# Kernel tuning notes

Hardware: AMD Instinct MI355X
Metric: run time of the kernel (lower is better)

The kernel has to match this reference:

```python
import jax, jax.numpy as jnp
import numpy as np
import math

EMBED_DIM = 1024
NUM_HEADS = 16
HEAD_DIM = EMBED_DIM // NUM_HEADS


def setup_inputs() -> dict:
    key = jax.random.key(0)
    ks = jax.random.split(key, 9)
    B, S, D = 4, 2048, EMBED_DIM
    s = 1.0 / math.sqrt(D)
    x = jax.random.normal(ks[0], (B, S, D), dtype=jnp.float32)
    Wq = jax.random.normal(ks[1], (D, D), dtype=jnp.float32) * s
    bq = jnp.zeros((D,), dtype=jnp.float32)
    Wk = jax.random.normal(ks[2], (D, D), dtype=jnp.float32) * s
    bk = jnp.zeros((D,), dtype=jnp.float32)
    Wv = jax.random.normal(ks[3], (D, D), dtype=jnp.float32) * s
    bv = jnp.zeros((D,), dtype=jnp.float32)
    Wo = jax.random.normal(ks[4], (D, D), dtype=jnp.float32) * s
    bo = jnp.zeros((D,), dtype=jnp.float32)
    return {"x": x, "Wq": Wq, "bq": bq, "Wk": Wk, "bk": bk,
            "Wv": Wv, "bv": bv, "Wo": Wo, "bo": bo}


def reference(x, Wq, bq, Wk, bk, Wv, bv, Wo, bo):
    B, S, D = x.shape
    H, hd = NUM_HEADS, HEAD_DIM
    # projections: [B,S,D] -> [B,H,S,hd]
    def split_heads(t):
        return t.reshape(B, S, H, hd).transpose(0, 2, 1, 3)
    Q = split_heads(x @ Wq + bq)
    K = split_heads(x @ Wk + bk)
    V = split_heads(x @ Wv + bv)
    scale = 1.0 / math.sqrt(hd)
    scores = jnp.einsum('bhqd,bhkd->bhqk', Q, K) * scale  # [B,H,S,S]
    causal = jnp.tril(jnp.ones((S, S), dtype=bool))
    scores = jnp.where(causal, scores, -jnp.inf)
    attn = jax.nn.softmax(scores, axis=-1)
    out = jnp.einsum('bhqk,bhkd->bhqd', attn, V)  # [B,H,S,hd]
    out = out.transpose(0, 2, 1, 3).reshape(B, S, D)
    return out @ Wo + bo
```

## Files before the change

kernel.cpp:

```cpp
#include <hip/hip_runtime.h>
#include <hip/hip_bf16.h>
#include <cstdint>
#include <cstddef>

typedef __bf16 bf16_t;
typedef __bf16 bf16x4 __attribute__((ext_vector_type(4)));
typedef __bf16 bf16x8 __attribute__((ext_vector_type(8)));
typedef float f32x4 __attribute__((ext_vector_type(4)));
typedef float f32x16 __attribute__((ext_vector_type(16)));
typedef unsigned u32x2 __attribute__((ext_vector_type(2)));

typedef __attribute__((address_space(1))) void as1_void_t;
typedef __attribute__((address_space(3))) void as3_void_t;

__device__ __forceinline__ void gload_lds16(const bf16_t* g, bf16_t* l) {
  __builtin_amdgcn_global_load_lds((as1_void_t*)g, (as3_void_t*)l, 16, 0, 0);
}

__global__ __launch_bounds__(256) void prep_x_k(
    const float* __restrict__ x, bf16_t* __restrict__ xb)
{
  const int stride = gridDim.x * blockDim.x;
  const int tid = blockIdx.x * blockDim.x + threadIdx.x;
  const int NX4 = (8192 * 1024) / 4;
  for (int i = tid; i < NX4; i += stride) {
    float4 v = ((const float4*)x)[i];
    bf16x4 o;
    o[0] = (bf16_t)v.x; o[1] = (bf16_t)v.y; o[2] = (bf16_t)v.z; o[3] = (bf16_t)v.w;
    ((bf16x4*)xb)[i] = o;
  }
}

__global__ __launch_bounds__(256) void prep_w_k(
    const float* __restrict__ wq, const float* __restrict__ wk,
    const float* __restrict__ wv, const float* __restrict__ wo,
    bf16_t* __restrict__ wqt, bf16_t* __restrict__ wkt,
    bf16_t* __restrict__ wvt, bf16_t* __restrict__ wot)
{
  __shared__ float t[64][65];
  const int zz = blockIdx.y;
  const float* w = (zz == 0) ? wq : (zz == 1) ? wk : (zz == 2) ? wv : wo;
  bf16_t* wt = (zz == 0) ? wqt : (zz == 1) ? wkt : (zz == 2) ? wvt : wot;
  const int tile = blockIdx.x;
  const int tr = tile >> 4, tc = tile & 15;
  const int c = threadIdx.x & 63, r4 = threadIdx.x >> 6;
#pragma unroll
  for (int rr = 0; rr < 16; ++rr) {
    int row = rr * 4 + r4;
    t[row][c] = w[(size_t)(tr * 64 + row) * 1024 + tc * 64 + c];
  }
  __syncthreads();
#pragma unroll
  for (int rr = 0; rr < 16; ++rr) {
    int row = rr * 4 + r4;
    wt[(size_t)(tc * 64 + row) * 1024 + tr * 64 + c] = (bf16_t)t[c][row];
  }
}

constexpr int BM = 128, BN = 128, BK = 64;

__global__ __launch_bounds__(256) void gemm_qkv_k(
    const bf16_t* __restrict__ A,
    const bf16_t* __restrict__ WqT, const bf16_t* __restrict__ WkT,
    const bf16_t* __restrict__ WvT,
    const float* __restrict__ bq, const float* __restrict__ bk,
    const float* __restrict__ bv,
    bf16_t* __restrict__ qo, bf16_t* __restrict__ ko, bf16_t* __restrict__ vo)
{
  constexpr int K = 1024;
  __shared__ bf16_t a_lds[BM * BK];
  __shared__ bf16_t b_lds[BN * BK];
  const int z = blockIdx.z;
  const bf16_t* Bt = (z == 0) ? WqT : (z == 1) ? WkT : WvT;
  const float* bias = (z == 0) ? bq : (z == 1) ? bk : bv;
  bf16_t* outp = (z == 0) ? qo : (z == 1) ? ko : vo;
  const float oscale = (z == 0) ? 0.18033688011112042f : 1.0f;

  const int tid = threadIdx.x;
  const int l = tid & 63;
  const int wv = tid >> 6;
  const int wr = wv >> 1, wc = wv & 1;
  const int lr = l & 15, lg = l >> 4;
  const int bm = blockIdx.x * BM;
  const int bn = blockIdx.y * BN;

  f32x4 acc[4][4] = {};

  const int srow = tid >> 3;
  const int scc = tid & 7;

  for (int k0 = 0; k0 < K; k0 += BK) {
    __syncthreads();
#pragma unroll
    for (int it = 0; it < 4; ++it) {
      int row = srow + it * 32;
      int gk = (scc ^ (row & 7)) * 8;
      gload_lds16(A + (size_t)(bm + row) * K + k0 + gk, a_lds + row * BK + scc * 8);
      gload_lds16(Bt + (size_t)(bn + row) * K + k0 + gk, b_lds + row * BK + scc * 8);
    }
    __syncthreads();
#pragma unroll
    for (int kk = 0; kk < 2; ++kk) {
      bf16x8 af[4], bfr[4];
#pragma unroll
      for (int m = 0; m < 4; ++m) {
        int row = wr * 64 + m * 16 + lr;
        int ch = (kk * 4 + lg) ^ (row & 7);
        af[m] = *(const bf16x8*)&a_lds[row * BK + ch * 8];
      }
#pragma unroll
      for (int n = 0; n < 4; ++n) {
        int row = wc * 64 + n * 16 + lr;
        int ch = (kk * 4 + lg) ^ (row & 7);
        bfr[n] = *(const bf16x8*)&b_lds[row * BK + ch * 8];
      }
#pragma unroll
      for (int m = 0; m < 4; ++m)
#pragma unroll
        for (int n = 0; n < 4; ++n)
          acc[m][n] = __builtin_amdgcn_mfma_f32_16x16x32_bf16(af[m], bfr[n], acc[m][n], 0, 0, 0);
    }
  }

#pragma unroll
  for (int m = 0; m < 4; ++m) {
#pragma unroll
    for (int n = 0; n < 4; ++n) {
#pragma unroll
      for (int r = 0; r < 4; ++r) {
        int row = bm + wr * 64 + m * 16 + lg * 4 + r;
        int col = bn + wc * 64 + n * 16 + lr;
        float v = acc[m][n][r] + bias[col];
        const int bh = (row >> 11) * 16 + (col >> 6);
        const int seq = row & 2047;
        const int d = col & 63;
        if (z < 2) {
          size_t off = (((size_t)(bh * 64 + (seq >> 5)) * 4 + (d >> 4)) * 64
                        + (((d >> 3) & 1) * 32 + (seq & 31))) * 8 + (d & 7);
          outp[off] = (bf16_t)(v * oscale);
        } else {
          size_t off = ((((size_t)(bh * 64 + (seq >> 5)) * 2 + (d >> 5)) * 2
                         + ((seq >> 4) & 1)) * 64
                        + (((seq >> 3) & 1) * 32 + (d & 31))) * 8 + (seq & 7);
          outp[off] = (bf16_t)v;
        }
      }
    }
  }
}

__global__ __launch_bounds__(256) void gemm_o_k(
    const bf16_t* __restrict__ A, const bf16_t* __restrict__ Bt,
    const float* __restrict__ bias, float* __restrict__ outp)
{
  constexpr int K = 1024;
  __shared__ bf16_t a_lds[BM * BK];
  __shared__ bf16_t b_lds[BN * BK];
  const int tid = threadIdx.x;
  const int l = tid & 63;
  const int wv = tid >> 6;
  const int wr = wv >> 1, wc = wv & 1;
  const int lr = l & 15, lg = l >> 4;
  const int bm = blockIdx.x * BM;
  const int bn = blockIdx.y * BN;

  f32x4 acc[4][4] = {};
  const int srow = tid >> 3;
  const int scc = tid & 7;

  for (int k0 = 0; k0 < K; k0 += BK) {
    __syncthreads();
#pragma unroll
    for (int it = 0; it < 4; ++it) {
      int row = srow + it * 32;
      int gk = (scc ^ (row & 7)) * 8;
      gload_lds16(A + (size_t)(bm + row) * K + k0 + gk, a_lds + row * BK + scc * 8);
      gload_lds16(Bt + (size_t)(bn + row) * K + k0 + gk, b_lds + row * BK + scc * 8);
    }
    __syncthreads();
#pragma unroll
    for (int kk = 0; kk < 2; ++kk) {
      bf16x8 af[4], bfr[4];
#pragma unroll
      for (int m = 0; m < 4; ++m) {
        int row = wr * 64 + m * 16 + lr;
        int ch = (kk * 4 + lg) ^ (row & 7);
        af[m] = *(const bf16x8*)&a_lds[row * BK + ch * 8];
      }
#pragma unroll
      for (int n = 0; n < 4; ++n) {
        int row = wc * 64 + n * 16 + lr;
        int ch = (kk * 4 + lg) ^ (row & 7);
        bfr[n] = *(const bf16x8*)&b_lds[row * BK + ch * 8];
      }
#pragma unroll
      for (int m = 0; m < 4; ++m)
#pragma unroll
        for (int n = 0; n < 4; ++n)
          acc[m][n] = __builtin_amdgcn_mfma_f32_16x16x32_bf16(af[m], bfr[n], acc[m][n], 0, 0, 0);
    }
  }

#pragma unroll
  for (int m = 0; m < 4; ++m)
#pragma unroll
    for (int n = 0; n < 4; ++n)
#pragma unroll
      for (int r = 0; r < 4; ++r) {
        int row = bm + wr * 64 + m * 16 + lg * 4 + r;
        int col = bn + wc * 64 + n * 16 + lr;
        outp[(size_t)row * 1024 + col] = acc[m][n][r] + bias[col];
      }
}

__device__ __forceinline__ unsigned pack2bf(float a, float b) {
  union { bf16_t h[2]; unsigned u; } z;
  z.h[0] = (bf16_t)a; z.h[1] = (bf16_t)b;
  return z.u;
}

__device__ __forceinline__ void permswap(unsigned& a, unsigned& b) {
  u32x2 r = __builtin_amdgcn_permlane32_swap(a, b, false, false);
  a = r[0]; b = r[1];
}

__device__ __forceinline__ float xadd32(float x) {
  unsigned a = __float_as_uint(x), b = __float_as_uint(x);
  permswap(a, b);
  return __uint_as_float(a) + __uint_as_float(b);
}

__device__ __forceinline__ void sm_pv(
    const f32x16& st, const bf16x8 vf[2][2], f32x16 oacc[2], float& ls)
{
  float p[16];
#pragma unroll
  for (int r = 0; r < 16; ++r) p[r] = __builtin_amdgcn_exp2f(st[r] - 16.0f);
  float s0 = (p[0] + p[1]) + (p[2] + p[3]);
  float s1 = (p[4] + p[5]) + (p[6] + p[7]);
  float s2 = (p[8] + p[9]) + (p[10] + p[11]);
  float s3 = (p[12] + p[13]) + (p[14] + p[15]);
  ls += ((s0 + s1) + (s2 + s3));

  bf16x8 pf[2];
#pragma unroll
  for (int ks = 0; ks < 2; ++ks) {
    unsigned a0 = pack2bf(p[8 * ks + 0], p[8 * ks + 1]);
    unsigned a1 = pack2bf(p[8 * ks + 2], p[8 * ks + 3]);
    unsigned b0 = pack2bf(p[8 * ks + 4], p[8 * ks + 5]);
    unsigned b1 = pack2bf(p[8 * ks + 6], p[8 * ks + 7]);
    permswap(a0, b0);
    permswap(a1, b1);
    union { unsigned wd[4]; bf16x8 v; } zz;
    zz.wd[0] = a0; zz.wd[1] = a1; zz.wd[2] = b0; zz.wd[3] = b1;
    pf[ks] = zz.v;
  }
  __builtin_amdgcn_s_setprio(1);
#pragma unroll
  for (int dt = 0; dt < 2; ++dt)
#pragma unroll
    for (int ks = 0; ks < 2; ++ks)
      oacc[dt] = __builtin_amdgcn_mfma_f32_32x32x16_bf16(vf[dt][ks], pf[ks], oacc[dt], 0, 0, 0);
  __builtin_amdgcn_s_setprio(0);
}

__global__ __launch_bounds__(256) void attn_k(
    const bf16_t* __restrict__ Q, const bf16_t* __restrict__ Kmat,
    const bf16_t* __restrict__ Vt, bf16_t* __restrict__ O)
{
  const int bh = blockIdx.x;
  const int tid = threadIdx.x;
  const int l = tid & 63;
  const int w = tid >> 6;
  const int idx = blockIdx.y * 4 + w;
  const int t1 = idx, t2 = 63 - idx;
  const int qb1 = t1 * 32, qb2 = t2 * 32;
  const int lc = l & 31;
  const int hi = l >> 5;

  const bf16_t* Qh = Q + (size_t)bh * 131072 + l * 8;
  const bf16_t* Kh = Kmat + (size_t)bh * 131072 + l * 8;
  const bf16_t* Vh = Vt + (size_t)bh * 131072 + l * 8;

  bf16x8 qf1[4], qf2[4];
#pragma unroll
  for (int ds = 0; ds < 4; ++ds) {
    qf1[ds] = *(const bf16x8*)&Qh[(size_t)(t1 * 4 + ds) * 512];
    qf2[ds] = *(const bf16x8*)&Qh[(size_t)(t2 * 4 + ds) * 512];
  }

  float ls1 = 0.f, ls2 = 0.f;
  f32x16 o1[2] = {}, o2[2] = {};

  auto step = [&](const bf16x8 (&kf)[4], bf16x8 (&kfn)[4], int kvt) {
    const bf16_t* vb = &Vh[(size_t)kvt * 2048];
    bf16x8 vf[2][2];
    vf[0][0] = *(const bf16x8*)&vb[0];
    vf[0][1] = *(const bf16x8*)&vb[512];
    vf[1][0] = *(const bf16x8*)&vb[1024];
    vf[1][1] = *(const bf16x8*)&vb[1536];
    const int kvn = (kvt + 1 <= t2) ? kvt + 1 : kvt;
#pragma unroll
    for (int ds = 0; ds < 4; ++ds)
      kfn[ds] = *(const bf16x8*)&Kh[(size_t)(kvn * 4 + ds) * 512];

    f32x16 st2 = {};
    __builtin_amdgcn_s_setprio(1);
#pragma unroll
    for (int ds = 0; ds < 4; ++ds)
      st2 = __builtin_amdgcn_mfma_f32_32x32x16_bf16(kf[ds], qf2[ds], st2, 0, 0, 0);
    __builtin_amdgcn_s_setprio(0);
    const bool d1 = (kvt <= t1);
    f32x16 st1 = {};
    if (d1) {
      __builtin_amdgcn_s_setprio(1);
#pragma unroll
      for (int ds = 0; ds < 4; ++ds)
        st1 = __builtin_amdgcn_mfma_f32_32x32x16_bf16(kf[ds], qf1[ds], st1, 0, 0, 0);
      __builtin_amdgcn_s_setprio(0);
    }
    if (kvt == t2) {
#pragma unroll
      for (int r = 0; r < 16; ++r) {
        int kvloc = (r & 3) + 8 * (r >> 2) + 4 * hi;
        if (kvloc > lc) st2[r] = -1e30f;
      }
    }
    if (d1 && kvt == t1) {
#pragma unroll
      for (int r = 0; r < 16; ++r) {
        int kvloc = (r & 3) + 8 * (r >> 2) + 4 * hi;
        if (kvloc > lc) st1[r] = -1e30f;
      }
    }
    sm_pv(st2, vf, o2, ls2);
    if (d1) sm_pv(st1, vf, o1, ls1);
  };

  bf16x8 kfA[4], kfB[4];
#pragma unroll
  for (int ds = 0; ds < 4; ++ds)
    kfA[ds] = *(const bf16x8*)&Kh[(size_t)ds * 512];

  int kvt = 0;
  while (true) {
    step(kfA, kfB, kvt);
    ++kvt;
    if (kvt > t2) break;
    step(kfB, kfA, kvt);
    ++kvt;
    if (kvt > t2) break;
  }

  const int b = bh >> 4, h = bh & 15;
  {
    const float inv = 1.0f / xadd32(ls1);
    const size_t rowoff = (size_t)(b * 2048 + qb1 + lc) * 1024 + h * 64;
#pragma unroll
    for (int dt = 0; dt < 2; ++dt)
#pragma unroll
      for (int g = 0; g < 4; ++g) {
        bf16x4 o4;
#pragma unroll
        for (int t = 0; t < 4; ++t) o4[t] = (bf16_t)(o1[dt][g * 4 + t] * inv);
        *(bf16x4*)&O[rowoff + dt * 32 + g * 8 + hi * 4] = o4;
      }
  }
  {
    const float inv = 1.0f / xadd32(ls2);
    const size_t rowoff = (size_t)(b * 2048 + qb2 + lc) * 1024 + h * 64;
#pragma unroll
    for (int dt = 0; dt < 2; ++dt)
#pragma unroll
      for (int g = 0; g < 4; ++g) {
        bf16x4 o4;
#pragma unroll
        for (int t = 0; t < 4; ++t) o4[t] = (bf16_t)(o2[dt][g * 4 + t] * inv);
        *(bf16x4*)&O[rowoff + dt * 32 + g * 8 + hi * 4] = o4;
      }
  }
}

extern "C" void kernel_launch(void* const* d_in, const int* in_sizes, int n_in,
                              void* d_out, int out_size, void* d_ws, size_t ws_size,
                              hipStream_t stream)
{
  (void)in_sizes; (void)n_in; (void)out_size; (void)ws_size;
  const float* x  = (const float*)d_in[0];
  const float* Wq = (const float*)d_in[1];
  const float* bq = (const float*)d_in[2];
  const float* Wk = (const float*)d_in[3];
  const float* bk = (const float*)d_in[4];
  const float* Wv = (const float*)d_in[5];
  const float* bv = (const float*)d_in[6];
  const float* Wo = (const float*)d_in[7];
  const float* bo = (const float*)d_in[8];

  char* ws = (char*)d_ws;
  bf16_t* xb   = (bf16_t*)(ws);
  bf16_t* wqt  = (bf16_t*)(ws + (size_t)(16u << 20));
  bf16_t* wkt  = (bf16_t*)(ws + (size_t)(18u << 20));
  bf16_t* wvt  = (bf16_t*)(ws + (size_t)(20u << 20));
  bf16_t* wot  = (bf16_t*)(ws + (size_t)(22u << 20));
  bf16_t* qws  = (bf16_t*)(ws + (size_t)(24u << 20));
  bf16_t* kws  = (bf16_t*)(ws + (size_t)(40u << 20));
  bf16_t* vtws = (bf16_t*)(ws + (size_t)(56u << 20));

  prep_x_k<<<2048, 256, 0, stream>>>(x, xb);
  prep_w_k<<<dim3(256, 4), 256, 0, stream>>>(Wq, Wk, Wv, Wo, wqt, wkt, wvt, wot);

  dim3 gg(8192 / BM, 1024 / BN, 3);
  gemm_qkv_k<<<gg, 256, 0, stream>>>(xb, wqt, wkt, wvt, bq, bk, bv, qws, kws, vtws);

  attn_k<<<dim3(64, 8), 256, 0, stream>>>(qws, kws, vtws, xb);

  dim3 go(8192 / BM, 1024 / BN);
  gemm_o_k<<<go, 256, 0, stream>>>(xb, wot, bo, (float*)d_out);
}
```

Baseline: 198.9 us.

## Share K/V tiles across waves via LDS with async multi-buffered staging

In the attention kernel, each wave used to load its own K and V fragments straight from global memory. Now the block cooperatively stages each K/V tile into a 4-slot LDS ring with global_load_lds and waits with vmcnt plus a barrier, so all four waves reuse one copy. This is meant to cut redundant global/L2 traffic and hide load latency by prefetching two tiles ahead. In exchange it adds a block-wide barrier every step, and waves with shorter ranges must idle through the iterations up to the block's maximum t2.

```diff
diff --git a/kernel.cpp b/kernel.cpp
--- a/kernel.cpp
+++ b/kernel.cpp
@@ -269,87 +269,95 @@
     const bf16_t* __restrict__ Vt, bf16_t* __restrict__ O)
 {
   const int bh = blockIdx.x;
+  const int by = blockIdx.y;
   const int tid = threadIdx.x;
   const int l = tid & 63;
   const int w = tid >> 6;
-  const int idx = blockIdx.y * 4 + w;
+  const int idx = by * 4 + w;
   const int t1 = idx, t2 = 63 - idx;
+  const int t2max = 63 - by * 4;
   const int qb1 = t1 * 32, qb2 = t2 * 32;
   const int lc = l & 31;
   const int hi = l >> 5;
 
-  const bf16_t* Qh = Q + (size_t)bh * 131072 + l * 8;
-  const bf16_t* Kh = Kmat + (size_t)bh * 131072 + l * 8;
-  const bf16_t* Vh = Vt + (size_t)bh * 131072 + l * 8;
+  __shared__ bf16_t kbuf[4][2048];
+  __shared__ bf16_t vbuf[4][2048];
+
+  const bf16_t* Kg = Kmat + (size_t)bh * 131072;
+  const bf16_t* Vg = Vt + (size_t)bh * 131072;
+  const bf16_t* Qf = Q + (size_t)bh * 131072 + l * 8;
 
   bf16x8 qf1[4], qf2[4];
 #pragma unroll
   for (int ds = 0; ds < 4; ++ds) {
-    qf1[ds] = *(const bf16x8*)&Qh[(size_t)(t1 * 4 + ds) * 512];
-    qf2[ds] = *(const bf16x8*)&Qh[(size_t)(t2 * 4 + ds) * 512];
+    qf1[ds] = *(const bf16x8*)&Qf[(size_t)(t1 * 4 + ds) * 512];
+    qf2[ds] = *(const bf16x8*)&Qf[(size_t)(t2 * 4 + ds) * 512];
   }
 
   float ls1 = 0.f, ls2 = 0.f;
   f32x16 o1[2] = {}, o2[2] = {};
 
-  auto step = [&](const bf16x8 (&kf)[4], bf16x8 (&kfn)[4], int kvt) {
-    const bf16_t* vb = &Vh[(size_t)kvt * 2048];
-    bf16x8 vf[2][2];
-    vf[0][0] = *(const bf16x8*)&vb[0];
-    vf[0][1] = *(const bf16x8*)&vb[512];
-    vf[1][0] = *(const bf16x8*)&vb[1024];
-    vf[1][1] = *(const bf16x8*)&vb[1536];
-    const int kvn = (kvt + 1 <= t2) ? kvt + 1 : kvt;
-#pragma unroll
-    for (int ds = 0; ds < 4; ++ds)
-      kfn[ds] = *(const bf16x8*)&Kh[(size_t)(kvn * 4 + ds) * 512];
-
-    f32x16 st2 = {};
-    __builtin_amdgcn_s_setprio(1);
-#pragma unroll
-    for (int ds = 0; ds < 4; ++ds)
-      st2 = __builtin_amdgcn_mfma_f32_32x32x16_bf16(kf[ds], qf2[ds], st2, 0, 0, 0);
-    __builtin_amdgcn_s_setprio(0);
-    const bool d1 = (kvt <= t1);
-    f32x16 st1 = {};
-    if (d1) {
+  auto stage = [&](int kvt, int slot) {
+    int c = (kvt <= t2max) ? kvt : t2max;
+    gload_lds16(Kg + (size_t)c * 2048 + tid * 8, &kbuf[slot][tid * 8]);
+    gload_lds16(Vg + (size_t)c * 2048 + tid * 8, &vbuf[slot][tid * 8]);
+  };
+
+  stage(0, 0);
+  stage(1, 1);
+
+  for (int s = 0; s <= t2max; ++s) {
+    stage(s + 2, (s + 2) & 3);
+    asm volatile("s_waitcnt vmcnt(4)" ::: "memory");
+    __builtin_amdgcn_s_barrier();
+    __builtin_amdgcn_sched_barrier(0);
+
+    const bool d2 = (s <= t2);
+    const bool d1 = (s <= t1);
+    if (d2) {
+      const bf16_t* kb = &kbuf[s & 3][l * 8];
+      const bf16_t* vb = &vbuf[s & 3][l * 8];
+      bf16x8 kf[4];
+#pragma unroll
+      for (int ds = 0; ds < 4; ++ds) kf[ds] = *(const bf16x8*)&kb[ds * 512];
+      bf16x8 vf[2][2];
+#pragma unroll
+      for (int dt = 0; dt < 2; ++dt)
+#pragma unroll
+        for (int ks = 0; ks < 2; ++ks)
+          vf[dt][ks] = *(const bf16x8*)&vb[(dt * 2 + ks) * 512];
+
+      f32x16 st2 = {};
       __builtin_amdgcn_s_setprio(1);
 #pragma unroll
       for (int ds = 0; ds < 4; ++ds)
-        st1 = __builtin_amdgcn_mfma_f32_32x32x16_bf16(kf[ds], qf1[ds], st1, 0, 0, 0);
+        st2 = __builtin_amdgcn_mfma_f32_32x32x16_bf16(kf[ds], qf2[ds], st2, 0, 0, 0);
       __builtin_amdgcn_s_setprio(0);
-    }
-    if (kvt == t2) {
-#pragma unroll
-      for (int r = 0; r < 16; ++r) {
-        int kvloc = (r & 3) + 8 * (r >> 2) + 4 * hi;
-        if (kvloc > lc) st2[r] = -1e30f;
-      }
-    }
-    if (d1 && kvt == t1) {
-#pragma unroll
-      for (int r = 0; r < 16; ++r) {
-        int kvloc = (r & 3) + 8 * (r >> 2) + 4 * hi;
-        if (kvloc > lc) st1[r] = -1e30f;
-      }
-    }
-    sm_pv(st2, vf, o2, ls2);
-    if (d1) sm_pv(st1, vf, o1, ls1);
-  };
-
-  bf16x8 kfA[4], kfB[4];
-#pragma unroll
-  for (int ds = 0; ds < 4; ++ds)
-    kfA[ds] = *(const bf16x8*)&Kh[(size_t)ds * 512];
-
-  int kvt = 0;
-  while (true) {
-    step(kfA, kfB, kvt);
-    ++kvt;
-    if (kvt > t2) break;
-    step(kfB, kfA, kvt);
-    ++kvt;
-    if (kvt > t2) break;
+      f32x16 st1 = {};
+      if (d1) {
+        __builtin_amdgcn_s_setprio(1);
+#pragma unroll
+        for (int ds = 0; ds < 4; ++ds)
+          st1 = __builtin_amdgcn_mfma_f32_32x32x16_bf16(kf[ds], qf1[ds], st1, 0, 0, 0);
+        __builtin_amdgcn_s_setprio(0);
+      }
+      if (s == t2) {
+#pragma unroll
+        for (int r = 0; r < 16; ++r) {
+          int kvloc = (r & 3) + 8 * (r >> 2) + 4 * hi;
+          if (kvloc > lc) st2[r] = -1e30f;
+        }
+      }
+      if (d1 && s == t1) {
+#pragma unroll
+        for (int r = 0; r < 16; ++r) {
+          int kvloc = (r & 3) + 8 * (r >> 2) + 4 * hi;
+          if (kvloc > lc) st1[r] = -1e30f;
+        }
+      }
+      sm_pv(st2, vf, o2, ls2);
+      if (d1) sm_pv(st1, vf, o1, ls1);
+    }
   }
 
   const int b = bh >> 4, h = bh & 15;
```

New measurement: 193.6 us. -2.7%, faster.
